# Performance work log

Measured on AMD Instinct MI355X. Metric: run time of the kernel, lower is better.

Reference implementation:

```python
import jax, jax.numpy as jnp
import numpy as np

D_X = 16
D_L = 8
T_LEN = 131072
BIN_THRES = 0.1


def setup_inputs() -> dict:
    key = jax.random.key(0)
    ks = jax.random.split(key, 24)
    n = lambda k, shp, sc=0.1: jax.random.normal(k, shp, jnp.float32) * sc
    inp = {
        "latent_mean": jax.random.normal(ks[0], (2, T_LEN, D_L), jnp.float32),
        "latent_logvar": jax.random.normal(ks[1], (2, T_LEN, D_L), jnp.float32),
        "T": jax.random.uniform(ks[2], (T_LEN, 1), jnp.float32),
        # curr_adj_encoder: MLP(1 -> d_L -> d_L -> d_L*d_X), lrelu
        "cw0": n(ks[3], (1, D_L)), "cb0": n(ks[4], (D_L,)),
        "cw1": n(ks[5], (D_L, D_L)), "cb1": n(ks[6], (D_L,)),
        "cw2": n(ks[7], (D_L, D_L * D_X)), "cb2": n(ks[8], (D_L * D_X,)),
        # pre_adj_encoder
        "pw0": n(ks[9], (1, D_L)), "pb0": n(ks[10], (D_L,)),
        "pw1": n(ks[11], (D_L, D_L)), "pb1": n(ks[12], (D_L,)),
        "pw2": n(ks[13], (D_L, D_L * D_X)), "pb2": n(ks[14], (D_L * D_X,)),
        # latent_mean_out: FeatureExtractor(d_L,128,relu) + Linear(128,d_L)
        "fmw1": n(ks[15], (D_L, 128)), "fmb1": jnp.zeros((128,), jnp.float32),
        "fmw2": n(ks[16], (128, D_L)), "fmb2": jnp.zeros((D_L,), jnp.float32),
        # latent_logvar_out
        "fvw1": n(ks[17], (D_L, 128)), "fvb1": jnp.zeros((128,), jnp.float32),
        "fvw2": n(ks[18], (128, D_L)), "fvb2": jnp.zeros((D_L,), jnp.float32),
        # L2M per-node MLPs, batched over d_X: 4*d_L -> 64 -> 64 -> 1
        "lw0": n(ks[19], (D_X, 4 * D_L, 64)), "lb0": jnp.zeros((D_X, 64), jnp.float32),
        "lw1": n(ks[20], (D_X, 64, 64)), "lb1": jnp.zeros((D_X, 64), jnp.float32),
        "lw2": n(ks[21], (D_X, 64, 1)), "lb2": jnp.zeros((D_X, 1), jnp.float32),
    }
    return inp


def _forward(latent_mean, latent_logvar, T,
             cw0, cb0, cw1, cb1, cw2, cb2,
             pw0, pb0, pw1, pb1, pw2, pb2,
             fmw1, fmb1, fmw2, fmb2,
             fvw1, fvb1, fvw2, fvb2,
             lw0, lb0, lw1, lb1, lw2, lb2):
    lrelu = jax.nn.leaky_relu

    def mlp(x, w0, b0, w1, b1, w2, b2):
        h = lrelu(x @ w0 + b0)
        h = lrelu(h @ w1 + b1)
        return h @ w2 + b2

    Ct = mlp(T, cw0, cb0, cw1, cb1, cw2, cb2).reshape(-1, D_X, D_L)
    Ct_1 = mlp(T, pw0, pb0, pw1, pb1, pw2, pb2).reshape(-1, D_X, D_L)
    # Only Ct is binarized in the original forward (Ct_1 stays continuous).
    Ct = jnp.where(Ct < BIN_THRES, 0.0, 1.0).astype(Ct.dtype)

    zeros = jnp.zeros_like(latent_mean[:, :1, :])
    lm_prev = jnp.concatenate([zeros, latent_mean[:, :-1, :]], axis=1)
    lv_prev = jnp.concatenate([zeros, latent_logvar[:, :-1, :]], axis=1)

    def head(x, w1, b1, w2, b2):
        return jax.nn.relu(x @ w1 + b1) @ w2 + b2

    lm_pred = head(latent_mean, fmw1, fmb1, fmw2, fmb2)
    lv_pred = head(latent_logvar, fvw1, fvb1, fvw2, fvb2)

    def decode(lm, lv, C):
        # C: [T, d_X, d_L]; lm/lv: [2, T, d_L]
        def gather(x):
            g = jnp.einsum('ijk,lik->lijk', C, x)          # [2, T, d_X, d_L]
            g = jnp.transpose(g, (1, 2, 3, 0))              # [T, d_X, d_L, 2]
            return g.reshape(x.shape[1], D_X, 2 * D_L)
        h = jnp.concatenate([gather(lm), gather(lv)], axis=-1)  # [T, d_X, 4*d_L]
        h = jax.nn.relu(jnp.einsum('tnf,nfo->tno', h, lw0) + lb0)
        h = jnp.einsum('tnf,nfo->tno', h, lw1) + lb1             # last decoder layer: no relu
        h = jnp.einsum('tnf,nfo->tno', h, lw2) + lb2             # [T, d_X, 1]
        return jax.nn.relu(h[..., 0])                             # [T, d_X]

    recon = decode(latent_mean, latent_logvar, Ct)
    pred = decode(lm_prev, lv_prev, Ct_1)
    return recon, pred, lm_pred, lv_pred, Ct, Ct_1


def reference(latent_mean, latent_logvar, T,
              cw0, cb0, cw1, cb1, cw2, cb2,
              pw0, pb0, pw1, pb1, pw2, pb2,
              fmw1, fmb1, fmw2, fmb2,
              fvw1, fvb1, fvw2, fvb2,
              lw0, lb0, lw1, lb1, lw2, lb2):
    return _forward(latent_mean, latent_logvar, T,
                    cw0, cb0, cw1, cb1, cw2, cb2,
                    pw0, pb0, pw1, pb1, pw2, pb2,
                    fmw1, fmb1, fmw2, fmb2,
                    fvw1, fvb1, fvw2, fvb2,
                    lw0, lb0, lw1, lb1, lw2, lb2)
```

## Files before the change

kernel.cpp:

```cpp
#include <hip/hip_runtime.h>
#include <math.h>

#define TL 131072

static constexpr size_t OFF_RECON = 0;
static constexpr size_t OFF_PRED  = (size_t)TL * 16;
static constexpr size_t OFF_LMP   = (size_t)TL * 32;
static constexpr size_t OFF_LVP   = (size_t)TL * 48;
static constexpr size_t OFF_CT    = (size_t)TL * 64;
static constexpr size_t OFF_CT1   = (size_t)TL * 192;

typedef _Float16 h2 __attribute__((ext_vector_type(2)));
typedef _Float16 h8 __attribute__((ext_vector_type(8)));
typedef float f32x4 __attribute__((ext_vector_type(4)));

struct Params {
  const float* lm;  const float* lv;  const float* Tin;
  const float* cw0; const float* cb0; const float* cw1; const float* cb1; const float* cw2; const float* cb2;
  const float* pw0; const float* pb0; const float* pw1; const float* pb1; const float* pw2; const float* pb2;
  const float* fmw1; const float* fmb1; const float* fmw2; const float* fmb2;
  const float* fvw1; const float* fvb1; const float* fvw2; const float* fvb2;
  const float* lw0; const float* lb0; const float* lw1; const float* lb1; const float* lw2; const float* lb2;
  const float* w12src;
  float* out;
};

__device__ __forceinline__ const float4* rc4(const float* p) { return reinterpret_cast<const float4*>(p); }
__device__ __forceinline__ float4*       rw4(float* p)       { return reinterpret_cast<float4*>(p); }

__device__ __forceinline__ void load8(const float* __restrict__ src, float* dst) {
  float4 a = rc4(src)[0], b = rc4(src)[1];
  dst[0]=a.x; dst[1]=a.y; dst[2]=a.z; dst[3]=a.w;
  dst[4]=b.x; dst[5]=b.y; dst[6]=b.z; dst[7]=b.w;
}
__device__ __forceinline__ void store8(float* __restrict__ dst, const float* v) {
  rw4(dst)[0] = make_float4(v[0],v[1],v[2],v[3]);
  rw4(dst)[1] = make_float4(v[4],v[5],v[6],v[7]);
}
__device__ __forceinline__ void store16(float* __restrict__ dst, const float* v) {
  rw4(dst)[0] = make_float4(v[0],v[1],v[2],v[3]);
  rw4(dst)[1] = make_float4(v[4],v[5],v[6],v[7]);
  rw4(dst)[2] = make_float4(v[8],v[9],v[10],v[11]);
  rw4(dst)[3] = make_float4(v[12],v[13],v[14],v[15]);
}

union U4 { uint32_t u[4]; h2 h[4]; h8 v; uint4 q; };

__device__ __forceinline__ h2 pack2(float a, float b) {
  h2 r; r[0] = (_Float16)a; r[1] = (_Float16)b; return r;
}

__global__ __launch_bounds__(256) void tld_prep(const float* __restrict__ lw1,
                                                const float* __restrict__ lw2,
                                                const float* __restrict__ lb1,
                                                const float* __restrict__ lb2,
                                                float* __restrict__ ws) {
  const int tid = threadIdx.x;
  #pragma unroll 1
  for (int i = tid; i < 1024; i += 256) {
    int n = i >> 6, h = i & 63;
    float s = 0.f;
    #pragma unroll 8
    for (int o = 0; o < 64; ++o)
      s = fmaf(lw1[n * 4096 + h * 64 + o], lw2[n * 64 + o], s);
    ws[i] = s;
  }
  if (tid < 16) {
    float b = lb2[tid];
    #pragma unroll 8
    for (int o = 0; o < 64; ++o)
      b = fmaf(lb1[tid * 64 + o], lw2[tid * 64 + o], b);
    ws[1024 + tid] = b;
  }
}

__global__ __launch_bounds__(256, 4) void tld_fused(Params p) {
  __shared__ __align__(16) _Float16 s_W[2][64 * 40];
  __shared__ __align__(16) float    s_w12[1024];
  __shared__ __align__(16) float    s_b12[16];
  __shared__ __align__(16) float    s_lb0[1024];
  __shared__ __align__(16) char     s_pool[22080];

  float* s_hw1t = (float*)s_pool;
  float* s_hw2  = (float*)(s_pool + 8192);
  float* s_hb1  = (float*)(s_pool + 16384);
  float* s_hb2  = (float*)(s_pool + 17408);
  float* s_ew2t = (float*)(s_pool + 17472);
  float* s_eb2b = (float*)(s_pool + 21568);
  _Float16* s_resh = (_Float16*)s_pool;

  const int tid = threadIdx.x;
  const int B   = blockIdx.x * 128;

  rw4(s_lb0)[tid]          = rc4(p.lb0)[tid];
  rw4(s_hw2)[tid]          = rc4(p.fmw2)[tid];
  rw4(s_hw2 + 1024)[tid]   = rc4(p.fvw2)[tid];
  if (tid < 32)       { rw4(s_hb1)[tid] = rc4(p.fmb1)[tid]; }
  else if (tid < 64)  { rw4(s_hb1 + 128)[tid - 32] = rc4(p.fvb1)[tid - 32]; }
  else if (tid < 96)  { rw4(s_eb2b)[tid - 64] = rc4(p.pb2)[tid - 64]; }
  else if (tid < 100) { int q = tid - 96; rw4(s_hb2 + (q >> 1) * 8)[q & 1] = rc4((q >> 1) ? p.fvb2 : p.fmb2)[q & 1]; }
  #pragma unroll 1
  for (int i = tid; i < 2048; i += 256) {
    int r = i >> 10, ii = i & 1023, o = ii >> 3, f = ii & 7;
    s_hw1t[r * 1024 + ii] = (r ? p.fvw1 : p.fmw1)[f * 128 + o];
  }
  if (tid < 128) {
    #pragma unroll
    for (int i = 0; i < 8; ++i) s_ew2t[tid * 8 + i] = p.pw2[i * 128 + tid];
  }
  if (p.w12src) {
    rw4(s_w12)[tid] = rc4(p.w12src)[tid];
    if (tid < 4) rw4(s_b12)[tid] = rc4(p.w12src + 1024)[tid];
  } else {
    #pragma unroll 1
    for (int i = tid; i < 1024; i += 256) {
      int n = i >> 6, h = i & 63;
      float s = 0.f;
      for (int o = 0; o < 64; ++o)
        s = fmaf(p.lw1[n * 4096 + h * 64 + o], p.lw2[n * 64 + o], s);
      s_w12[i] = s;
    }
    if (tid < 16) {
      float b = p.lb2[tid];
      for (int o = 0; o < 64; ++o)
        b = fmaf(p.lb1[tid * 64 + o], p.lw2[tid * 64 + o], b);
      s_b12[tid] = b;
    }
  }
  const int wk  = tid & 31;
  const int wj0 = (tid >> 5) * 8;
  {
    const float4* g = rc4(p.lw0);
    float4 wa = g[wk * 16 + (tid >> 5) * 2];
    float4 wb = g[wk * 16 + (tid >> 5) * 2 + 1];
    _Float16* dW = s_W[0];
    dW[(wj0 + 0) * 40 + wk] = (_Float16)wa.x;
    dW[(wj0 + 1) * 40 + wk] = (_Float16)wa.y;
    dW[(wj0 + 2) * 40 + wk] = (_Float16)wa.z;
    dW[(wj0 + 3) * 40 + wk] = (_Float16)wa.w;
    dW[(wj0 + 4) * 40 + wk] = (_Float16)wb.x;
    dW[(wj0 + 5) * 40 + wk] = (_Float16)wb.y;
    dW[(wj0 + 6) * 40 + wk] = (_Float16)wb.z;
    dW[(wj0 + 7) * 40 + wk] = (_Float16)wb.w;
  }
  __syncthreads();

  const int u    = tid & 127;
  const int t    = B + u;
  const int role = __builtin_amdgcn_readfirstlane((int)(tid >> 7));
  const float Tt = p.Tin[t];

  if (role == 0) {
    double e0d[8], e1d[8];
    const double Td = (double)Tt;
    #pragma unroll
    for (int j = 0; j < 8; ++j) {
      double v = Td * (double)p.cw0[j] + (double)p.cb0[j];
      e0d[j] = v < 0.0 ? 0.01 * v : v;
    }
    #pragma unroll
    for (int j = 0; j < 8; ++j) {
      double v = (double)p.cb1[j];
      #pragma unroll
      for (int i = 0; i < 8; ++i) v = fma(e0d[i], (double)p.cw1[i * 8 + j], v);
      e1d[j] = v < 0.0 ? 0.01 * v : v;
    }
    #pragma unroll 1
    for (int n2 = 0; n2 < 8; ++n2) {
      float cb[16];
      #pragma unroll
      for (int kk = 0; kk < 16; ++kk) {
        const int nk = n2 * 16 + kk;
        double s = (double)p.cb2[nk];
        #pragma unroll
        for (int i = 0; i < 8; ++i)
          s = fma(e1d[i], (double)p.cw2[i * 128 + nk], s);
        cb[kk] = (s < 0.1) ? 0.f : 1.f;
      }
      store16(p.out + OFF_CT + (size_t)t * 128 + n2 * 16, cb);
    }
  } else {
    float e0[8], e1f[8];
    #pragma unroll
    for (int j = 0; j < 8; ++j) {
      float v = fmaf(Tt, p.pw0[j], p.pb0[j]);
      e0[j] = v < 0.f ? 0.01f * v : v;
    }
    #pragma unroll
    for (int j = 0; j < 8; ++j) {
      float v = p.pb1[j];
      #pragma unroll
      for (int i = 0; i < 8; ++i) v = fmaf(e0[i], p.pw1[i * 8 + j], v);
      e1f[j] = v < 0.f ? 0.01f * v : v;
    }
    #pragma unroll 1
    for (int n2 = 0; n2 < 8; ++n2) {
      float cb[16];
      #pragma unroll
      for (int kk = 0; kk < 16; ++kk) {
        const int nk = n2 * 16 + kk;
        const float4* w = (const float4*)&s_ew2t[nk * 8];
        float4 x0 = w[0], x1 = w[1];
        float s = s_eb2b[nk];
        s = fmaf(e1f[0], x0.x, s); s = fmaf(e1f[1], x0.y, s);
        s = fmaf(e1f[2], x0.z, s); s = fmaf(e1f[3], x0.w, s);
        s = fmaf(e1f[4], x1.x, s); s = fmaf(e1f[5], x1.y, s);
        s = fmaf(e1f[6], x1.z, s); s = fmaf(e1f[7], x1.w, s);
        cb[kk] = s;
      }
      store16(p.out + OFF_CT1 + (size_t)t * 128 + n2 * 16, cb);
    }
  }

  {
    float hx[2][8];
    if (role == 0) {
      load8(p.lm + (size_t)t * 8, hx[0]);
      load8(p.lm + (size_t)TL * 8 + (size_t)t * 8, hx[1]);
    } else {
      load8(p.lv + (size_t)t * 8, hx[0]);
      load8(p.lv + (size_t)TL * 8 + (size_t)t * 8, hx[1]);
    }
    const float* w1t  = s_hw1t + role * 1024;
    const float* w2r  = s_hw2  + role * 1024;
    const float* b1   = s_hb1  + role * 128;
    const float* hb2r = s_hb2  + role * 8;
    float acc8[2][8];
    #pragma unroll
    for (int l = 0; l < 2; ++l)
      #pragma unroll
      for (int j = 0; j < 8; ++j) acc8[l][j] = hb2r[j];
    #pragma unroll 1
    for (int o = 0; o < 128; ++o) {
      float4 u0 = rc4(w1t)[o * 2], u1 = rc4(w1t)[o * 2 + 1];
      const float wf[8] = {u0.x,u0.y,u0.z,u0.w,u1.x,u1.y,u1.z,u1.w};
      const float bo = b1[o];
      float a0 = bo, a1 = bo;
      #pragma unroll
      for (int f = 0; f < 8; ++f) {
        a0 = fmaf(hx[0][f], wf[f], a0);
        a1 = fmaf(hx[1][f], wf[f], a1);
      }
      a0 = fmaxf(a0, 0.f); a1 = fmaxf(a1, 0.f);
      float4 v0 = rc4(w2r)[o * 2], v1 = rc4(w2r)[o * 2 + 1];
      const float w2f[8] = {v0.x,v0.y,v0.z,v0.w,v1.x,v1.y,v1.z,v1.w};
      #pragma unroll
      for (int j = 0; j < 8; ++j) {
        acc8[0][j] = fmaf(a0, w2f[j], acc8[0][j]);
        acc8[1][j] = fmaf(a1, w2f[j], acc8[1][j]);
      }
    }
    const size_t hbase = role ? OFF_LVP : OFF_LMP;
    store8(p.out + hbase + (size_t)t * 8, acc8[0]);
    store8(p.out + hbase + (size_t)TL * 8 + (size_t)t * 8, acc8[1]);
  }

  __syncthreads();

  const int w     = tid >> 6;
  const int lane  = tid & 63;
  const int drole = __builtin_amdgcn_readfirstlane(w >> 1);
  const int tl0   = (w & 1) * 64;
  const int l15   = lane & 15;
  const int g     = lane >> 4;
  const int kb    = (g & 1) * 4;
  const float* xbase = (g < 2) ? p.lm : p.lv;
  const float* Cbuf  = p.out + (drole ? OFF_CT1 : OFF_CT);
  _Float16* resw = s_resh + w * 1088;

  int trow[4];
  U4 dv[4];
  #pragma unroll
  for (int ti = 0; ti < 4; ++ti) {
    trow[ti] = B + tl0 + ti * 16 + l15;
    const int src = trow[ti] - drole;
    const int s0  = src < 0 ? 0 : src;
    float4 v0 = rc4(xbase + (size_t)s0 * 8 + kb)[0];
    float4 v1 = rc4(xbase + (size_t)TL * 8 + (size_t)s0 * 8 + kb)[0];
    U4 dd;
    dd.h[0] = pack2(v0.x, v1.x);
    dd.h[1] = pack2(v0.y, v1.y);
    dd.h[2] = pack2(v0.z, v1.z);
    dd.h[3] = pack2(v0.w, v1.w);
    if (src < 0) dd.q = make_uint4(0u, 0u, 0u, 0u);
    dv[ti] = dd;
  }

  #pragma unroll 1
  for (int n = 0; n < 16; ++n) {
    float4 wa, wb;
    if (n < 15) {
      const float4* gsrc = rc4(p.lw0 + (size_t)(n + 1) * 2048);
      wa = gsrc[wk * 16 + (tid >> 5) * 2];
      wb = gsrc[wk * 16 + (tid >> 5) * 2 + 1];
    }
    const _Float16* Wcur = s_W[n & 1];
    h8 Af0 = *(const h8*)&Wcur[( 0 + l15) * 40 + g * 8];
    h8 Af1 = *(const h8*)&Wcur[(16 + l15) * 40 + g * 8];
    h8 Af2 = *(const h8*)&Wcur[(32 + l15) * 40 + g * 8];
    h8 Af3 = *(const h8*)&Wcur[(48 + l15) * 40 + g * 8];
    const float b12n = s_b12[n];

    #pragma unroll
    for (int ti = 0; ti < 4; ++ti) {
      float4 cc = rc4(Cbuf + (size_t)trow[ti] * 128 + n * 8 + kb)[0];
      U4 bx;
      bx.h[0] = pack2(cc.x, cc.x) * dv[ti].h[0];
      bx.h[1] = pack2(cc.y, cc.y) * dv[ti].h[1];
      bx.h[2] = pack2(cc.z, cc.z) * dv[ti].h[2];
      bx.h[3] = pack2(cc.w, cc.w) * dv[ti].h[3];
      const h8 Bf = bx.v;

      float partial = 0.f;
      {
        float4 bias = rc4(s_lb0 + n * 64 +  0 + g * 4)[0];
        f32x4 d; d[0]=bias.x; d[1]=bias.y; d[2]=bias.z; d[3]=bias.w;
        d = __builtin_amdgcn_mfma_f32_16x16x32_f16(Af0, Bf, d, 0, 0, 0);
        float4 wv = rc4(s_w12 + n * 64 +  0 + g * 4)[0];
        partial = fmaf(fmaxf(d[0],0.f), wv.x, partial);
        partial = fmaf(fmaxf(d[1],0.f), wv.y, partial);
        partial = fmaf(fmaxf(d[2],0.f), wv.z, partial);
        partial = fmaf(fmaxf(d[3],0.f), wv.w, partial);
      }
      {
        float4 bias = rc4(s_lb0 + n * 64 + 16 + g * 4)[0];
        f32x4 d; d[0]=bias.x; d[1]=bias.y; d[2]=bias.z; d[3]=bias.w;
        d = __builtin_amdgcn_mfma_f32_16x16x32_f16(Af1, Bf, d, 0, 0, 0);
        float4 wv = rc4(s_w12 + n * 64 + 16 + g * 4)[0];
        partial = fmaf(fmaxf(d[0],0.f), wv.x, partial);
        partial = fmaf(fmaxf(d[1],0.f), wv.y, partial);
        partial = fmaf(fmaxf(d[2],0.f), wv.z, partial);
        partial = fmaf(fmaxf(d[3],0.f), wv.w, partial);
      }
      {
        float4 bias = rc4(s_lb0 + n * 64 + 32 + g * 4)[0];
        f32x4 d; d[0]=bias.x; d[1]=bias.y; d[2]=bias.z; d[3]=bias.w;
        d = __builtin_amdgcn_mfma_f32_16x16x32_f16(Af2, Bf, d, 0, 0, 0);
        float4 wv = rc4(s_w12 + n * 64 + 32 + g * 4)[0];
        partial = fmaf(fmaxf(d[0],0.f), wv.x, partial);
        partial = fmaf(fmaxf(d[1],0.f), wv.y, partial);
        partial = fmaf(fmaxf(d[2],0.f), wv.z, partial);
        partial = fmaf(fmaxf(d[3],0.f), wv.w, partial);
      }
      {
        float4 bias = rc4(s_lb0 + n * 64 + 48 + g * 4)[0];
        f32x4 d; d[0]=bias.x; d[1]=bias.y; d[2]=bias.z; d[3]=bias.w;
        d = __builtin_amdgcn_mfma_f32_16x16x32_f16(Af3, Bf, d, 0, 0, 0);
        float4 wv = rc4(s_w12 + n * 64 + 48 + g * 4)[0];
        partial = fmaf(fmaxf(d[0],0.f), wv.x, partial);
        partial = fmaf(fmaxf(d[1],0.f), wv.y, partial);
        partial = fmaf(fmaxf(d[2],0.f), wv.z, partial);
        partial = fmaf(fmaxf(d[3],0.f), wv.w, partial);
      }
      partial += __shfl_xor(partial, 16, 64);
      partial += __shfl_xor(partial, 32, 64);
      const float r = fmaxf(b12n + partial, 0.f);
      if (lane < 16) resw[n * 68 + ti * 16 + l15] = (_Float16)r;
    }

    if (n < 15) {
      _Float16* dW = s_W[(n + 1) & 1];
      dW[(wj0 + 0) * 40 + wk] = (_Float16)wa.x;
      dW[(wj0 + 1) * 40 + wk] = (_Float16)wa.y;
      dW[(wj0 + 2) * 40 + wk] = (_Float16)wa.z;
      dW[(wj0 + 3) * 40 + wk] = (_Float16)wa.w;
      dW[(wj0 + 4) * 40 + wk] = (_Float16)wb.x;
      dW[(wj0 + 5) * 40 + wk] = (_Float16)wb.y;
      dW[(wj0 + 6) * 40 + wk] = (_Float16)wb.z;
      dW[(wj0 + 7) * 40 + wk] = (_Float16)wb.w;
    }
    __syncthreads();
  }

  {
    float o16[16];
    #pragma unroll
    for (int n = 0; n < 16; ++n) o16[n] = (float)resw[n * 68 + lane];
    const size_t r_off = drole ? OFF_PRED : OFF_RECON;
    store16(p.out + r_off + (size_t)(B + tl0 + lane) * 16, o16);
  }
}

extern "C" void kernel_launch(void* const* d_in, const int* in_sizes, int n_in,
                              void* d_out, int out_size, void* d_ws, size_t ws_size,
                              hipStream_t stream) {
  Params p;
  p.lm   = (const float*)d_in[0];
  p.lv   = (const float*)d_in[1];
  p.Tin  = (const float*)d_in[2];
  p.cw0  = (const float*)d_in[3];  p.cb0 = (const float*)d_in[4];
  p.cw1  = (const float*)d_in[5];  p.cb1 = (const float*)d_in[6];
  p.cw2  = (const float*)d_in[7];  p.cb2 = (const float*)d_in[8];
  p.pw0  = (const float*)d_in[9];  p.pb0 = (const float*)d_in[10];
  p.pw1  = (const float*)d_in[11]; p.pb1 = (const float*)d_in[12];
  p.pw2  = (const float*)d_in[13]; p.pb2 = (const float*)d_in[14];
  p.fmw1 = (const float*)d_in[15]; p.fmb1 = (const float*)d_in[16];
  p.fmw2 = (const float*)d_in[17]; p.fmb2 = (const float*)d_in[18];
  p.fvw1 = (const float*)d_in[19]; p.fvb1 = (const float*)d_in[20];
  p.fvw2 = (const float*)d_in[21]; p.fvb2 = (const float*)d_in[22];
  p.lw0  = (const float*)d_in[23]; p.lb0 = (const float*)d_in[24];
  p.lw1  = (const float*)d_in[25]; p.lb1 = (const float*)d_in[26];
  p.lw2  = (const float*)d_in[27]; p.lb2 = (const float*)d_in[28];
  p.out  = (float*)d_out;

  const bool use_ws = ws_size >= 1040 * sizeof(float);
  if (use_ws) {
    tld_prep<<<dim3(1), dim3(256), 0, stream>>>(p.lw1, p.lw2, p.lb1, p.lb2, (float*)d_ws);
    p.w12src = (const float*)d_ws;
  } else {
    p.w12src = nullptr;
  }
  tld_fused<<<dim3(TL / 128), dim3(256), 0, stream>>>(p);
}
```

Measured before the change: 469.4 us.

## Split fused kernel into phase1 and persistent per-node decode kernel

Splits the single fused kernel into two launches. The first computes the adjacency encoders and the latent heads. The second is a persistent 1024-thread decode kernel in which each wave owns one node, so its layer-0 weights, biases and folded w12 vectors stay in registers across a grid-stride loop over 64-row chunks. This removes the per-node double-buffered LDS weight staging and its 16 block barriers per tile. In exchange, the decode kernel reloads the latent inputs for every node from global or cache memory, re-reads Ct/Ct_1 through global memory after a kernel boundary, and adds a second launch.

```diff
diff --git a/kernel.cpp b/kernel.cpp
--- a/kernel.cpp
+++ b/kernel.cpp
@@ -74,74 +74,31 @@
   }
 }
 
-__global__ __launch_bounds__(256, 4) void tld_fused(Params p) {
-  __shared__ __align__(16) _Float16 s_W[2][64 * 40];
-  __shared__ __align__(16) float    s_w12[1024];
-  __shared__ __align__(16) float    s_b12[16];
-  __shared__ __align__(16) float    s_lb0[1024];
-  __shared__ __align__(16) char     s_pool[22080];
-
-  float* s_hw1t = (float*)s_pool;
-  float* s_hw2  = (float*)(s_pool + 8192);
-  float* s_hb1  = (float*)(s_pool + 16384);
-  float* s_hb2  = (float*)(s_pool + 17408);
-  float* s_ew2t = (float*)(s_pool + 17472);
-  float* s_eb2b = (float*)(s_pool + 21568);
-  _Float16* s_resh = (_Float16*)s_pool;
+__global__ __launch_bounds__(256, 4) void tld_phase1(Params p) {
+  __shared__ __align__(16) float s_hw1t[2][1024];
+  __shared__ __align__(16) float s_hw2[2][1024];
+  __shared__ __align__(16) float s_hb1[2][128];
+  __shared__ __align__(16) float s_hb2[2][8];
+  __shared__ __align__(16) float s_ew2t[128 * 8];
+  __shared__ __align__(16) float s_eb2b[128];
 
   const int tid = threadIdx.x;
   const int B   = blockIdx.x * 128;
 
-  rw4(s_lb0)[tid]          = rc4(p.lb0)[tid];
-  rw4(s_hw2)[tid]          = rc4(p.fmw2)[tid];
-  rw4(s_hw2 + 1024)[tid]   = rc4(p.fvw2)[tid];
-  if (tid < 32)       { rw4(s_hb1)[tid] = rc4(p.fmb1)[tid]; }
-  else if (tid < 64)  { rw4(s_hb1 + 128)[tid - 32] = rc4(p.fvb1)[tid - 32]; }
+  rw4(&s_hw2[0][0])[tid] = rc4(p.fmw2)[tid];
+  rw4(&s_hw2[1][0])[tid] = rc4(p.fvw2)[tid];
+  if (tid < 32)       { rw4(&s_hb1[0][0])[tid] = rc4(p.fmb1)[tid]; }
+  else if (tid < 64)  { rw4(&s_hb1[1][0])[tid - 32] = rc4(p.fvb1)[tid - 32]; }
   else if (tid < 96)  { rw4(s_eb2b)[tid - 64] = rc4(p.pb2)[tid - 64]; }
-  else if (tid < 100) { int q = tid - 96; rw4(s_hb2 + (q >> 1) * 8)[q & 1] = rc4((q >> 1) ? p.fvb2 : p.fmb2)[q & 1]; }
+  else if (tid < 100) { int q = tid - 96; rw4(&s_hb2[q >> 1][0])[q & 1] = rc4((q >> 1) ? p.fvb2 : p.fmb2)[q & 1]; }
   #pragma unroll 1
   for (int i = tid; i < 2048; i += 256) {
     int r = i >> 10, ii = i & 1023, o = ii >> 3, f = ii & 7;
-    s_hw1t[r * 1024 + ii] = (r ? p.fvw1 : p.fmw1)[f * 128 + o];
+    s_hw1t[r][ii] = (r ? p.fvw1 : p.fmw1)[f * 128 + o];
   }
   if (tid < 128) {
     #pragma unroll
     for (int i = 0; i < 8; ++i) s_ew2t[tid * 8 + i] = p.pw2[i * 128 + tid];
-  }
-  if (p.w12src) {
-    rw4(s_w12)[tid] = rc4(p.w12src)[tid];
-    if (tid < 4) rw4(s_b12)[tid] = rc4(p.w12src + 1024)[tid];
-  } else {
-    #pragma unroll 1
-    for (int i = tid; i < 1024; i += 256) {
-      int n = i >> 6, h = i & 63;
-      float s = 0.f;
-      for (int o = 0; o < 64; ++o)
-        s = fmaf(p.lw1[n * 4096 + h * 64 + o], p.lw2[n * 64 + o], s);
-      s_w12[i] = s;
-    }
-    if (tid < 16) {
-      float b = p.lb2[tid];
-      for (int o = 0; o < 64; ++o)
-        b = fmaf(p.lb1[tid * 64 + o], p.lw2[tid * 64 + o], b);
-      s_b12[tid] = b;
-    }
-  }
-  const int wk  = tid & 31;
-  const int wj0 = (tid >> 5) * 8;
-  {
-    const float4* g = rc4(p.lw0);
-    float4 wa = g[wk * 16 + (tid >> 5) * 2];
-    float4 wb = g[wk * 16 + (tid >> 5) * 2 + 1];
-    _Float16* dW = s_W[0];
-    dW[(wj0 + 0) * 40 + wk] = (_Float16)wa.x;
-    dW[(wj0 + 1) * 40 + wk] = (_Float16)wa.y;
-    dW[(wj0 + 2) * 40 + wk] = (_Float16)wa.z;
-    dW[(wj0 + 3) * 40 + wk] = (_Float16)wa.w;
-    dW[(wj0 + 4) * 40 + wk] = (_Float16)wb.x;
-    dW[(wj0 + 5) * 40 + wk] = (_Float16)wb.y;
-    dW[(wj0 + 6) * 40 + wk] = (_Float16)wb.z;
-    dW[(wj0 + 7) * 40 + wk] = (_Float16)wb.w;
   }
   __syncthreads();
 
@@ -221,10 +178,10 @@
       load8(p.lv + (size_t)t * 8, hx[0]);
       load8(p.lv + (size_t)TL * 8 + (size_t)t * 8, hx[1]);
     }
-    const float* w1t  = s_hw1t + role * 1024;
-    const float* w2r  = s_hw2  + role * 1024;
-    const float* b1   = s_hb1  + role * 128;
-    const float* hb2r = s_hb2  + role * 8;
+    const float* w1t  = &s_hw1t[role][0];
+    const float* w2r  = &s_hw2[role][0];
+    const float* b1   = &s_hb1[role][0];
+    const float* hb2r = &s_hb2[role][0];
     float acc8[2][8];
     #pragma unroll
     for (int l = 0; l < 2; ++l)
@@ -254,130 +211,128 @@
     store8(p.out + hbase + (size_t)t * 8, acc8[0]);
     store8(p.out + hbase + (size_t)TL * 8 + (size_t)t * 8, acc8[1]);
   }
-
-  __syncthreads();
-
-  const int w     = tid >> 6;
-  const int lane  = tid & 63;
-  const int drole = __builtin_amdgcn_readfirstlane(w >> 1);
-  const int tl0   = (w & 1) * 64;
-  const int l15   = lane & 15;
-  const int g     = lane >> 4;
-  const int kb    = (g & 1) * 4;
+}
+
+__global__ __launch_bounds__(1024, 4) void tld_decode(Params p) {
+  __shared__ float s_res[16][68];
+
+  const int tid  = threadIdx.x;
+  const int n    = tid >> 6;
+  const int lane = tid & 63;
+  const int l15  = lane & 15;
+  const int g    = lane >> 4;
+  const int kb   = (g & 1) * 4;
   const float* xbase = (g < 2) ? p.lm : p.lv;
-  const float* Cbuf  = p.out + (drole ? OFF_CT1 : OFF_CT);
-  _Float16* resw = s_resh + w * 1088;
-
-  int trow[4];
-  U4 dv[4];
-  #pragma unroll
-  for (int ti = 0; ti < 4; ++ti) {
-    trow[ti] = B + tl0 + ti * 16 + l15;
-    const int src = trow[ti] - drole;
-    const int s0  = src < 0 ? 0 : src;
-    float4 v0 = rc4(xbase + (size_t)s0 * 8 + kb)[0];
-    float4 v1 = rc4(xbase + (size_t)TL * 8 + (size_t)s0 * 8 + kb)[0];
-    U4 dd;
-    dd.h[0] = pack2(v0.x, v1.x);
-    dd.h[1] = pack2(v0.y, v1.y);
-    dd.h[2] = pack2(v0.z, v1.z);
-    dd.h[3] = pack2(v0.w, v1.w);
-    if (src < 0) dd.q = make_uint4(0u, 0u, 0u, 0u);
-    dv[ti] = dd;
+
+  h8 Af0, Af1, Af2, Af3;
+  {
+    const float* wn = p.lw0 + (size_t)n * 2048;
+    h8 a0, a1, a2, a3;
+    #pragma unroll
+    for (int e = 0; e < 8; ++e) {
+      const float* col = wn + (g * 8 + e) * 64 + l15;
+      a0[e] = (_Float16)col[0];
+      a1[e] = (_Float16)col[16];
+      a2[e] = (_Float16)col[32];
+      a3[e] = (_Float16)col[48];
+    }
+    Af0 = a0; Af1 = a1; Af2 = a2; Af3 = a3;
+  }
+  const float4 bias0 = rc4(p.lb0 + n * 64 +  0 + g * 4)[0];
+  const float4 bias1 = rc4(p.lb0 + n * 64 + 16 + g * 4)[0];
+  const float4 bias2 = rc4(p.lb0 + n * 64 + 32 + g * 4)[0];
+  const float4 bias3 = rc4(p.lb0 + n * 64 + 48 + g * 4)[0];
+  float4 w0, w1, w2, w3; float b12n;
+  if (p.w12src) {
+    w0 = rc4(p.w12src + n * 64 +  0 + g * 4)[0];
+    w1 = rc4(p.w12src + n * 64 + 16 + g * 4)[0];
+    w2 = rc4(p.w12src + n * 64 + 32 + g * 4)[0];
+    w3 = rc4(p.w12src + n * 64 + 48 + g * 4)[0];
+    b12n = p.w12src[1024 + n];
+  } else {
+    const float* l2 = p.lw2 + n * 64;
+    float acc[16];
+    #pragma unroll
+    for (int q = 0; q < 4; ++q)
+      #pragma unroll
+      for (int r = 0; r < 4; ++r) {
+        const float* row = p.lw1 + (size_t)n * 4096 + (q * 16 + g * 4 + r) * 64;
+        float s = 0.f;
+        #pragma unroll 8
+        for (int o = 0; o < 64; ++o) s = fmaf(row[o], l2[o], s);
+        acc[q * 4 + r] = s;
+      }
+    w0 = make_float4(acc[0], acc[1], acc[2], acc[3]);
+    w1 = make_float4(acc[4], acc[5], acc[6], acc[7]);
+    w2 = make_float4(acc[8], acc[9], acc[10], acc[11]);
+    w3 = make_float4(acc[12], acc[13], acc[14], acc[15]);
+    float b = p.lb2[n];
+    #pragma unroll 8
+    for (int o = 0; o < 64; ++o) b = fmaf(p.lb1[n * 64 + o], l2[o], b);
+    b12n = b;
   }
 
   #pragma unroll 1
-  for (int n = 0; n < 16; ++n) {
-    float4 wa, wb;
-    if (n < 15) {
-      const float4* gsrc = rc4(p.lw0 + (size_t)(n + 1) * 2048);
-      wa = gsrc[wk * 16 + (tid >> 5) * 2];
-      wb = gsrc[wk * 16 + (tid >> 5) * 2 + 1];
-    }
-    const _Float16* Wcur = s_W[n & 1];
-    h8 Af0 = *(const h8*)&Wcur[( 0 + l15) * 40 + g * 8];
-    h8 Af1 = *(const h8*)&Wcur[(16 + l15) * 40 + g * 8];
-    h8 Af2 = *(const h8*)&Wcur[(32 + l15) * 40 + g * 8];
-    h8 Af3 = *(const h8*)&Wcur[(48 + l15) * 40 + g * 8];
-    const float b12n = s_b12[n];
+  for (int c = blockIdx.x; c < 4096; c += gridDim.x) {
+    const int role = c >> 11;
+    const int t0   = (c & 2047) << 6;
+    const float* Cbuf = p.out + (role ? OFF_CT1 : OFF_CT);
 
     #pragma unroll
     for (int ti = 0; ti < 4; ++ti) {
-      float4 cc = rc4(Cbuf + (size_t)trow[ti] * 128 + n * 8 + kb)[0];
+      const int trow = t0 + ti * 16 + l15;
+      const int src  = trow - role;
+      float4 v0 = make_float4(0.f, 0.f, 0.f, 0.f), v1 = v0;
+      if (src >= 0) {
+        v0 = rc4(xbase + (size_t)src * 8 + kb)[0];
+        v1 = rc4(xbase + (size_t)TL * 8 + (size_t)src * 8 + kb)[0];
+      }
+      const float4 cc = rc4(Cbuf + (size_t)trow * 128 + n * 8 + kb)[0];
       U4 bx;
-      bx.h[0] = pack2(cc.x, cc.x) * dv[ti].h[0];
-      bx.h[1] = pack2(cc.y, cc.y) * dv[ti].h[1];
-      bx.h[2] = pack2(cc.z, cc.z) * dv[ti].h[2];
-      bx.h[3] = pack2(cc.w, cc.w) * dv[ti].h[3];
+      bx.h[0] = pack2(cc.x * v0.x, cc.x * v1.x);
+      bx.h[1] = pack2(cc.y * v0.y, cc.y * v1.y);
+      bx.h[2] = pack2(cc.z * v0.z, cc.z * v1.z);
+      bx.h[3] = pack2(cc.w * v0.w, cc.w * v1.w);
       const h8 Bf = bx.v;
 
       float partial = 0.f;
-      {
-        float4 bias = rc4(s_lb0 + n * 64 +  0 + g * 4)[0];
-        f32x4 d; d[0]=bias.x; d[1]=bias.y; d[2]=bias.z; d[3]=bias.w;
+      { f32x4 d; d[0]=bias0.x; d[1]=bias0.y; d[2]=bias0.z; d[3]=bias0.w;
         d = __builtin_amdgcn_mfma_f32_16x16x32_f16(Af0, Bf, d, 0, 0, 0);
-        float4 wv = rc4(s_w12 + n * 64 +  0 + g * 4)[0];
-        partial = fmaf(fmaxf(d[0],0.f), wv.x, partial);
-        partial = fmaf(fmaxf(d[1],0.f), wv.y, partial);
-        partial = fmaf(fmaxf(d[2],0.f), wv.z, partial);
-        partial = fmaf(fmaxf(d[3],0.f), wv.w, partial);
-      }
-      {
-        float4 bias = rc4(s_lb0 + n * 64 + 16 + g * 4)[0];
-        f32x4 d; d[0]=bias.x; d[1]=bias.y; d[2]=bias.z; d[3]=bias.w;
+        partial = fmaf(fmaxf(d[0],0.f), w0.x, partial);
+        partial = fmaf(fmaxf(d[1],0.f), w0.y, partial);
+        partial = fmaf(fmaxf(d[2],0.f), w0.z, partial);
+        partial = fmaf(fmaxf(d[3],0.f), w0.w, partial); }
+      { f32x4 d; d[0]=bias1.x; d[1]=bias1.y; d[2]=bias1.z; d[3]=bias1.w;
         d = __builtin_amdgcn_mfma_f32_16x16x32_f16(Af1, Bf, d, 0, 0, 0);
-        float4 wv = rc4(s_w12 + n * 64 + 16 + g * 4)[0];
-        partial = fmaf(fmaxf(d[0],0.f), wv.x, partial);
-        partial = fmaf(fmaxf(d[1],0.f), wv.y, partial);
-        partial = fmaf(fmaxf(d[2],0.f), wv.z, partial);
-        partial = fmaf(fmaxf(d[3],0.f), wv.w, partial);
-      }
-      {
-        float4 bias = rc4(s_lb0 + n * 64 + 32 + g * 4)[0];
-        f32x4 d; d[0]=bias.x; d[1]=bias.y; d[2]=bias.z; d[3]=bias.w;
+        partial = fmaf(fmaxf(d[0],0.f), w1.x, partial);
+        partial = fmaf(fmaxf(d[1],0.f), w1.y, partial);
+        partial = fmaf(fmaxf(d[2],0.f), w1.z, partial);
+        partial = fmaf(fmaxf(d[3],0.f), w1.w, partial); }
+      { f32x4 d; d[0]=bias2.x; d[1]=bias2.y; d[2]=bias2.z; d[3]=bias2.w;
         d = __builtin_amdgcn_mfma_f32_16x16x32_f16(Af2, Bf, d, 0, 0, 0);
-        float4 wv = rc4(s_w12 + n * 64 + 32 + g * 4)[0];
-        partial = fmaf(fmaxf(d[0],0.f), wv.x, partial);
-        partial = fmaf(fmaxf(d[1],0.f), wv.y, partial);
-        partial = fmaf(fmaxf(d[2],0.f), wv.z, partial);
-        partial = fmaf(fmaxf(d[3],0.f), wv.w, partial);
-      }
-      {
-        float4 bias = rc4(s_lb0 + n * 64 + 48 + g * 4)[0];
-        f32x4 d; d[0]=bias.x; d[1]=bias.y; d[2]=bias.z; d[3]=bias.w;
+        partial = fmaf(fmaxf(d[0],0.f), w2.x, partial);
+        partial = fmaf(fmaxf(d[1],0.f), w2.y, partial);
+        partial = fmaf(fmaxf(d[2],0.f), w2.z, partial);
+        partial = fmaf(fmaxf(d[3],0.f), w2.w, partial); }
+      { f32x4 d; d[0]=bias3.x; d[1]=bias3.y; d[2]=bias3.z; d[3]=bias3.w;
         d = __builtin_amdgcn_mfma_f32_16x16x32_f16(Af3, Bf, d, 0, 0, 0);
-        float4 wv = rc4(s_w12 + n * 64 + 48 + g * 4)[0];
-        partial = fmaf(fmaxf(d[0],0.f), wv.x, partial);
-        partial = fmaf(fmaxf(d[1],0.f), wv.y, partial);
-        partial = fmaf(fmaxf(d[2],0.f), wv.z, partial);
-        partial = fmaf(fmaxf(d[3],0.f), wv.w, partial);
-      }
+        partial = fmaf(fmaxf(d[0],0.f), w3.x, partial);
+        partial = fmaf(fmaxf(d[1],0.f), w3.y, partial);
+        partial = fmaf(fmaxf(d[2],0.f), w3.z, partial);
+        partial = fmaf(fmaxf(d[3],0.f), w3.w, partial); }
+
       partial += __shfl_xor(partial, 16, 64);
       partial += __shfl_xor(partial, 32, 64);
       const float r = fmaxf(b12n + partial, 0.f);
-      if (lane < 16) resw[n * 68 + ti * 16 + l15] = (_Float16)r;
-    }
-
-    if (n < 15) {
-      _Float16* dW = s_W[(n + 1) & 1];
-      dW[(wj0 + 0) * 40 + wk] = (_Float16)wa.x;
-      dW[(wj0 + 1) * 40 + wk] = (_Float16)wa.y;
-      dW[(wj0 + 2) * 40 + wk] = (_Float16)wa.z;
-      dW[(wj0 + 3) * 40 + wk] = (_Float16)wa.w;
-      dW[(wj0 + 4) * 40 + wk] = (_Float16)wb.x;
-      dW[(wj0 + 5) * 40 + wk] = (_Float16)wb.y;
-      dW[(wj0 + 6) * 40 + wk] = (_Float16)wb.z;
-      dW[(wj0 + 7) * 40 + wk] = (_Float16)wb.w;
+      if (lane < 16) s_res[n][ti * 16 + l15] = r;
     }
     __syncthreads();
-  }
-
-  {
-    float o16[16];
-    #pragma unroll
-    for (int n = 0; n < 16; ++n) o16[n] = (float)resw[n * 68 + lane];
-    const size_t r_off = drole ? OFF_PRED : OFF_RECON;
-    store16(p.out + r_off + (size_t)(B + tl0 + lane) * 16, o16);
+    {
+      const int rr = tid >> 4, nn = tid & 15;
+      const size_t r_off = role ? OFF_PRED : OFF_RECON;
+      p.out[r_off + (size_t)(t0 + rr) * 16 + nn] = s_res[nn][rr];
+    }
+    __syncthreads();
   }
 }
 
@@ -410,5 +365,6 @@
   } else {
     p.w12src = nullptr;
   }
-  tld_fused<<<dim3(TL / 128), dim3(256), 0, stream>>>(p);
-}
+  tld_phase1<<<dim3(TL / 128), dim3(256), 0, stream>>>(p);
+  tld_decode<<<dim3(512), dim3(1024), 0, stream>>>(p);
+}
```

New measurement: 477.1 us. No clear change (+1.6%).
